# Kernel optimization log

Measured on AMD Instinct MI355X. Metric: run time of the kernel, lower is better.

Reference implementation:

```python
import jax, jax.numpy as jnp
import numpy as np

N_NODES = 50000
N_EDGES = 800000
F_IN = 64
HID = 256
N_GRAPHS = 128
N_OUT = 24


def _sage_conv(x, src, dst, deg_inv, wl, bl, wr):
    # PyG SAGEConv (aggr='mean'): out = lin_l(mean_{j in N(i)} x_j) + lin_r(x_i)
    agg = jax.ops.segment_sum(x[src], dst, num_segments=x.shape[0]) * deg_inv
    return agg @ wl.T + bl + x @ wr.T


def setup_inputs() -> dict:
    key = jax.random.key(0)
    ks = jax.random.split(key, 16)
    x = jax.random.normal(ks[0], (N_NODES, F_IN), dtype=jnp.float32)
    edge_index = jax.random.randint(ks[1], (2, N_EDGES), 0, N_NODES, dtype=jnp.int64)
    batch = jnp.sort(jax.random.randint(ks[2], (N_NODES,), 0, N_GRAPHS, dtype=jnp.int64))

    def lin(k, fan_out, fan_in):
        bound = 1.0 / np.sqrt(fan_in)
        return jax.random.uniform(k, (fan_out, fan_in), jnp.float32, -bound, bound)

    inp = {
        'x': x, 'edge_index': edge_index, 'batch': batch,
        'w1l': lin(ks[3], HID, F_IN), 'b1': jnp.zeros((HID,), jnp.float32), 'w1r': lin(ks[4], HID, F_IN),
        'w2l': lin(ks[5], HID, HID), 'b2': jnp.zeros((HID,), jnp.float32), 'w2r': lin(ks[6], HID, HID),
        'w3l': lin(ks[7], HID, HID), 'b3': jnp.zeros((HID,), jnp.float32), 'w3r': lin(ks[8], HID, HID),
        'lin1_w': lin(ks[9], HID // 2, HID), 'lin1_b': jnp.zeros((HID // 2,), jnp.float32),
        'lin2_w': lin(ks[10], N_OUT, HID // 2), 'lin2_b': jnp.zeros((N_OUT,), jnp.float32),
    }
    return inp


def reference(x, edge_index, batch, w1l, b1, w1r, w2l, b2, w2r, w3l, b3, w3r,
              lin1_w, lin1_b, lin2_w, lin2_b):
    src, dst = edge_index[0], edge_index[1]
    deg = jax.ops.segment_sum(jnp.ones((src.shape[0],), jnp.float32), dst, num_segments=x.shape[0])
    deg_inv = (1.0 / jnp.maximum(deg, 1.0))[:, None]  # [N,1]

    h = jax.nn.relu(_sage_conv(x, src, dst, deg_inv, w1l, b1, w1r))
    h = jax.nn.relu(_sage_conv(h, src, dst, deg_inv, w2l, b2, w2r))
    h = jax.nn.relu(_sage_conv(h, src, dst, deg_inv, w3l, b3, w3r))

    # global mean pool over graphs
    pooled_sum = jax.ops.segment_sum(h, batch, num_segments=N_GRAPHS)
    counts = jax.ops.segment_sum(jnp.ones((h.shape[0],), jnp.float32), batch, num_segments=N_GRAPHS)
    pooled = pooled_sum / jnp.maximum(counts, 1.0)[:, None]

    g = jax.nn.relu(pooled @ lin1_w.T + lin1_b)
    return g @ lin2_w.T + lin2_b
```

## Files before the change

kernel.cpp:

```cpp
#include <hip/hip_runtime.h>

#define N_NODES 50000
#define M_PAD   50048
#define N_EDGES 800000
#define F_IN 64
#define HID 256
#define N_GRAPHS 128
#define N_OUT 24

typedef unsigned short ushort_t;
typedef __attribute__((ext_vector_type(8))) unsigned short us8;
typedef __attribute__((ext_vector_type(8))) __bf16 bf16x8;
typedef __attribute__((ext_vector_type(4))) float f32x4;

#define SLICE_US ((size_t)M_PAD * 32)

__device__ __forceinline__ unsigned short f2bf(float f) {
  unsigned u = __builtin_bit_cast(unsigned, f);
  return (unsigned short)((u + 0x7fffu + ((u >> 16) & 1u)) >> 16);
}
__device__ __forceinline__ float bf2f(unsigned short h) {
  return __builtin_bit_cast(float, (unsigned)h << 16);
}

__device__ __forceinline__ f32x4 mfma_bf16(us8 a, us8 b, f32x4 c) {
  return __builtin_amdgcn_mfma_f32_16x16x32_bf16(
      __builtin_bit_cast(bf16x8, a), __builtin_bit_cast(bf16x8, b), c, 0, 0, 0);
}

__device__ __forceinline__ void gload16(const ushort_t* g, ushort_t* l) {
  __builtin_amdgcn_global_load_lds(
      (const __attribute__((address_space(1))) void*)g,
      (__attribute__((address_space(3))) void*)l, 16, 0, 0);
}


__global__ void k_hist(const int* __restrict__ dst, int* __restrict__ deg_priv,
                       int* __restrict__ rank) {
  int e = blockIdx.x * 256 + threadIdx.x;
  if (e < N_EDGES) {
    int c = blockIdx.x & 7;
    rank[e] = atomicAdd(&deg_priv[c * N_NODES + dst[e]], 1);
  }
}

__global__ void k_gofs(const int* __restrict__ batch, int* __restrict__ gofs) {
  int t = threadIdx.x;
  if (t > N_GRAPHS) return;
  int lo = 0, hi = N_NODES;
  while (lo < hi) {
    int mid = (lo + hi) >> 1;
    if (batch[mid] < t) lo = mid + 1;
    else hi = mid;
  }
  gofs[t] = lo;
}

__global__ __launch_bounds__(1024) void k_scan1(int* __restrict__ deg_priv,
                                                int* __restrict__ deg,
                                                int* __restrict__ rowptr,
                                                int* __restrict__ partial) {
  __shared__ int s[1024];
  int t = threadIdx.x;
  int idx = blockIdx.x * 1024 + t;
  int v = 0;
  if (idx < N_NODES) {
    int run = 0;
#pragma unroll
    for (int c = 0; c < 8; ++c) {
      int dv = deg_priv[c * N_NODES + idx];
      deg_priv[c * N_NODES + idx] = run;
      run += dv;
    }
    deg[idx] = run;
    v = run;
  }
  s[t] = v;
  __syncthreads();
  for (int off = 1; off < 1024; off <<= 1) {
    int a = (t >= off) ? s[t - off] : 0;
    __syncthreads();
    s[t] += a;
    __syncthreads();
  }
  if (idx < N_NODES) rowptr[idx] = s[t] - v;
  if (t == 1023) partial[blockIdx.x] = s[1023];
}

__global__ void k_scan2(int* __restrict__ partial, int* __restrict__ rowptr) {
  __shared__ int s[64];
  int t = threadIdx.x;
  const int NB = (N_NODES + 1023) / 1024;
  int v = (t < NB) ? partial[t] : 0;
  s[t] = v;
  __syncthreads();
  for (int off = 1; off < 64; off <<= 1) {
    int a = (t >= off) ? s[t - off] : 0;
    __syncthreads();
    s[t] += a;
    __syncthreads();
  }
  if (t < NB) partial[t] = s[t] - v;
  if (t == NB - 1) rowptr[N_NODES] = s[t];
}

__global__ __launch_bounds__(1024) void k_scan3(const int* __restrict__ deg,
                                                const int* __restrict__ partial,
                                                int* __restrict__ rowptr,
                                                float* __restrict__ deg_inv) {
  int idx = blockIdx.x * 1024 + threadIdx.x;
  if (idx < N_NODES) {
    rowptr[idx] += partial[blockIdx.x];
    deg_inv[idx] = 1.0f / fmaxf((float)deg[idx], 1.0f);
  }
}

__global__ void k_place(const int* __restrict__ src, const int* __restrict__ dst,
                        const int* __restrict__ rowptr, const int* __restrict__ deg_priv,
                        const int* __restrict__ rank, int* __restrict__ esrc) {
  int e = blockIdx.x * 256 + threadIdx.x;
  if (e < N_EDGES) {
    int c = blockIdx.x & 7;
    int d = dst[e];
    esrc[rowptr[d] + deg_priv[c * N_NODES + d] + rank[e]] = src[e];
  }
}


__global__ void k_prep_x(const float* __restrict__ x, ushort_t* __restrict__ xio) {
  int g = blockIdx.x * 256 + threadIdx.x;
  if (g >= N_NODES * 8) return;
  int row = g >> 3, kb = g & 7;
  const float* p = x + (size_t)row * F_IN + kb * 8;
  us8 H, L;
#pragma unroll
  for (int i = 0; i < 8; ++i) {
    float f = p[i];
    unsigned short hi = f2bf(f);
    H[i] = hi;
    L[i] = f2bf(f - bf2f(hi));
  }
  size_t ob = (size_t)row * 128 + (size_t)((kb ^ (row & 7)) << 3);
  *(us8*)&xio[ob] = H;
  *(us8*)&xio[ob + 64] = L;
}

__global__ void k_prep_w(const float* __restrict__ w1lp, const float* __restrict__ w1rp,
                         const float* __restrict__ w2lp, const float* __restrict__ w2rp,
                         const float* __restrict__ w3lp, const float* __restrict__ w3rp,
                         ushort_t* __restrict__ wf1, ushort_t* __restrict__ wf2,
                         ushort_t* __restrict__ wf3) {
  int layer = blockIdx.z, side = blockIdx.y;
  const int Kg = (layer == 0) ? 8 : 32;
  const int qcs = Kg >> 2;
  int g = blockIdx.x * 256 + threadIdx.x;
  if (g >= 256 * Kg) return;
  const float* src = (layer == 0) ? (side ? w1rp : w1lp)
                   : (layer == 1) ? (side ? w2rp : w2lp)
                                  : (side ? w3rp : w3lp);
  ushort_t* dstf = (layer == 0) ? wf1 : (layer == 1) ? wf2 : wf3;
  int row = g / Kg, gb = g % Kg;
  const float* p = src + (size_t)row * (Kg * 8) + gb * 8;
  us8 H, L;
#pragma unroll
  for (int i = 0; i < 8; ++i) {
    float f = p[i];
    unsigned short hi = f2bf(f);
    H[i] = hi;
    L[i] = f2bf(f - bf2f(hi));
  }
  int nb2 = side * 16 + (row >> 4);
  int lane = (row & 15) + ((gb & 3) << 4);
  size_t base = ((size_t)(nb2 * qcs + (gb >> 2)) * 2) * 512 + lane * 8;
  *(us8*)&dstf[base] = H;
  *(us8*)&dstf[base + 512] = L;
}


__global__ __launch_bounds__(256) void k_agg64s(const float* __restrict__ x,
                                                const int* __restrict__ rowptr,
                                                const int* __restrict__ esrc,
                                                const float* __restrict__ deg_inv,
                                                ushort_t* __restrict__ oio) {
  int node = blockIdx.x * 4 + (threadIdx.x >> 6);
  if (node >= N_NODES) return;
  int lane = threadIdx.x & 63;
  int e0 = rowptr[node], e1 = rowptr[node + 1];
  float acc = 0.f;
  int e = e0;
#pragma unroll 1
  for (; e + 8 <= e1; e += 8) {
    int sidx[8];
#pragma unroll
    for (int j = 0; j < 8; ++j) sidx[j] = esrc[e + j];
    float v[8];
#pragma unroll
    for (int j = 0; j < 8; ++j) v[j] = x[(size_t)sidx[j] * F_IN + lane];
    acc += ((v[0] + v[1]) + (v[2] + v[3])) + ((v[4] + v[5]) + (v[6] + v[7]));
  }
  if (e + 4 <= e1) {
    int s0 = esrc[e], s1 = esrc[e + 1], s2 = esrc[e + 2], s3 = esrc[e + 3];
    float v0 = x[(size_t)s0 * F_IN + lane];
    float v1 = x[(size_t)s1 * F_IN + lane];
    float v2 = x[(size_t)s2 * F_IN + lane];
    float v3 = x[(size_t)s3 * F_IN + lane];
    acc += (v0 + v1) + (v2 + v3);
    e += 4;
  }
  for (; e < e1; ++e) acc += x[(size_t)esrc[e] * F_IN + lane];
  acc *= deg_inv[node];
  unsigned short hi = f2bf(acc);
  unsigned short lo = f2bf(acc - bf2f(hi));
  size_t rb = (size_t)node * 128;
  int slot = ((lane >> 3) ^ (node & 7)) << 3;
  oio[rb + slot + (lane & 7)] = hi;
  oio[rb + 64 + slot + (lane & 7)] = lo;
}

__global__ __launch_bounds__(256) void k_agg256s(const ushort_t* __restrict__ hio,
                                                 const int* __restrict__ rowptr,
                                                 const int* __restrict__ esrc,
                                                 const float* __restrict__ deg_inv,
                                                 ushort_t* __restrict__ oio) {
  int c = blockIdx.x & 7;
  const ushort_t* hs = hio + (size_t)c * SLICE_US;
  ushort_t* os = oio + (size_t)c * SLICE_US;
  int q = threadIdx.x & 3;
  int ns = threadIdx.x >> 2;
  for (int base = (blockIdx.x >> 3) * 64; base < N_NODES; base += 16384) {
    int node = base + ns;
    if (node >= N_NODES) continue;
    int e0 = rowptr[node], e1 = rowptr[node + 1];
    float a[8] = {0.f, 0.f, 0.f, 0.f, 0.f, 0.f, 0.f, 0.f};
    int e = e0;
#pragma unroll 1
    for (; e + 8 <= e1; e += 8) {
      int sidx[8];
#pragma unroll
      for (int j = 0; j < 8; ++j) sidx[j] = esrc[e + j];
      us8 v[8];
#pragma unroll
      for (int j = 0; j < 8; ++j)
        v[j] = *(const us8*)&hs[(size_t)sidx[j] * 32 + ((q ^ (sidx[j] & 3)) << 3)];
#pragma unroll
      for (int j = 0; j < 8; ++j)
#pragma unroll
        for (int i = 0; i < 8; ++i) a[i] += bf2f(v[j][i]);
    }
    if (e + 4 <= e1) {
      int s0 = esrc[e], s1 = esrc[e + 1], s2 = esrc[e + 2], s3 = esrc[e + 3];
      us8 v0 = *(const us8*)&hs[(size_t)s0 * 32 + ((q ^ (s0 & 3)) << 3)];
      us8 v1 = *(const us8*)&hs[(size_t)s1 * 32 + ((q ^ (s1 & 3)) << 3)];
      us8 v2 = *(const us8*)&hs[(size_t)s2 * 32 + ((q ^ (s2 & 3)) << 3)];
      us8 v3 = *(const us8*)&hs[(size_t)s3 * 32 + ((q ^ (s3 & 3)) << 3)];
#pragma unroll
      for (int i = 0; i < 8; ++i)
        a[i] += (bf2f(v0[i]) + bf2f(v1[i])) + (bf2f(v2[i]) + bf2f(v3[i]));
      e += 4;
    }
    for (; e < e1; ++e) {
      int s = esrc[e];
      us8 v = *(const us8*)&hs[(size_t)s * 32 + ((q ^ (s & 3)) << 3)];
#pragma unroll
      for (int i = 0; i < 8; ++i) a[i] += bf2f(v[i]);
    }
    float di = deg_inv[node];
    us8 H;
#pragma unroll
    for (int i = 0; i < 8; ++i) H[i] = f2bf(a[i] * di);
    __builtin_nontemporal_store(
        H, (us8*)&os[(size_t)node * 32 + ((q ^ (node & 3)) << 3)]);
  }
}


template <int SA>
__global__ __launch_bounds__(256, 2) void k_gemm_mfma(
    const ushort_t* __restrict__ A1, int k1g, const ushort_t* __restrict__ w1f,
    const ushort_t* __restrict__ A2, int k2g, const ushort_t* __restrict__ w2f,
    const float* __restrict__ bias, ushort_t* __restrict__ oio,
    float* __restrict__ ofp, int mode) {
  __shared__ __align__(16) ushort_t ldsA[2][SA ? 16384 : 8192];

  int t = threadIdx.x;
  int wv = t >> 6, lane = t & 63;
  int fr = lane & 15, kq = lane >> 4;
  int bm = blockIdx.x;
  int rowA0 = bm * 128;

  f32x4 acc[8][4];
#pragma unroll
  for (int m = 0; m < 8; ++m)
#pragma unroll
    for (int n = 0; n < 4; ++n) acc[m][n] = (f32x4)0.f;

  const int ns1 = k1g >> 3, ns2 = k2g >> 3, ns = ns1 + ns2;
  const int lj = lane & 7, lr8 = lane >> 3;

  auto stage = [&](int buf, int s) {
    bool p2 = s >= ns1;
    const ushort_t* A = p2 ? A2 : A1;
    int Kg = p2 ? k2g : k1g;
    int sl = p2 ? (s - ns1) : s;
#pragma unroll
    for (int i = 0; i < 4; ++i) {
      int row = wv * 32 + i * 8 + lr8;
      int R = rowA0 + row;
      int lo = (wv * 32 + i * 8) * 64;
      if (SA) {
        size_t offA = ((size_t)R * (Kg * 2) + sl * 8 + lj) * 8;
        gload16(A + offA, &ldsA[buf][lo]);
        gload16(A + offA + (size_t)Kg * 8, &ldsA[buf][8192 + lo]);
      } else {
        size_t offA = (size_t)(sl * 2 + ((lj >> 2) ^ ((R >> 2) & 1))) * SLICE_US +
                      (size_t)R * 32 + (size_t)((lj & 3) << 3);
        gload16(A + offA, &ldsA[buf][lo]);
      }
    }
  };

  stage(0, 0);
  __syncthreads();
  int cur = 0;

  for (int s = 0; s < ns; ++s) {
    bool p2 = s >= ns1;
    const ushort_t* Wf = p2 ? w2f : w1f;
    int sl = p2 ? (s - ns1) : s;
    int qcs = (p2 ? k2g : k1g) >> 2;

    us8 bh[2][4], bl[2][4];
#pragma unroll
    for (int kc = 0; kc < 2; ++kc)
#pragma unroll
      for (int n = 0; n < 4; ++n) {
        size_t base = ((size_t)((wv * 4 + n) * qcs + sl * 2 + kc) * 2) * 512 + lane * 8;
        bh[kc][n] = *(const us8*)&Wf[base];
        bl[kc][n] = *(const us8*)&Wf[base + 512];
      }

    if (s + 1 < ns) stage(cur ^ 1, s + 1);

#pragma unroll
    for (int kc = 0; kc < 2; ++kc) {
      int kg = kc * 4 + kq;
      int swk = (kg ^ (fr & 7)) << 3;
#pragma unroll
      for (int mh = 0; mh < 2; ++mh) {
        us8 ah[4], al[4];
#pragma unroll
        for (int m = 0; m < 4; ++m) {
          int off = ((mh * 64 + m * 16 + fr) << 6) + swk;
          ah[m] = *(const us8*)&ldsA[cur][off];
          if (SA) al[m] = *(const us8*)&ldsA[cur][8192 + off];
        }
#pragma unroll
        for (int m = 0; m < 4; ++m)
#pragma unroll
          for (int n = 0; n < 4; ++n)
            acc[mh * 4 + m][n] = mfma_bf16(ah[m], bh[kc][n], acc[mh * 4 + m][n]);
#pragma unroll
        for (int m = 0; m < 4; ++m)
#pragma unroll
          for (int n = 0; n < 4; ++n)
            acc[mh * 4 + m][n] = mfma_bf16(ah[m], bl[kc][n], acc[mh * 4 + m][n]);
        if (SA) {
#pragma unroll
          for (int m = 0; m < 4; ++m)
#pragma unroll
            for (int n = 0; n < 4; ++n)
              acc[mh * 4 + m][n] = mfma_bf16(al[m], bh[kc][n], acc[mh * 4 + m][n]);
        }
      }
    }
    __syncthreads();
    cur ^= 1;
  }

  float bv4[4];
#pragma unroll
  for (int n = 0; n < 4; ++n) bv4[n] = bias[wv * 64 + n * 16 + fr];

  if (mode == 0) {
    ushort_t* eb = &ldsA[0][0] + wv * 2048;
#pragma unroll
    for (int c = 0; c < 4; ++c) {
      __syncthreads();
#pragma unroll
      for (int mm = 0; mm < 2; ++mm) {
#pragma unroll
        for (int n = 0; n < 4; ++n) {
          f32x4 v = acc[c * 2 + mm][n];
#pragma unroll
          for (int r = 0; r < 4; ++r)
            eb[(mm * 16 + kq * 4 + r) * 64 + n * 16 + fr] =
                f2bf(fmaxf(v[r] + bv4[n], 0.f));
        }
      }
      __syncthreads();
#pragma unroll
      for (int j = 0; j < 4; ++j) {
        int rl = j * 8 + (lane >> 3);
        int g8 = lane & 7;
        us8 v = *(const us8*)&eb[rl * 64 + g8 * 8];
        int R = bm * 128 + c * 32 + rl;
        int gi = wv * 8 + g8;
        if (R < N_NODES) {
          size_t addr = (size_t)(gi >> 2) * SLICE_US + (size_t)R * 32 +
                        (size_t)(((gi & 3) ^ (R & 3)) << 3);
          *(us8*)&oio[addr] = v;
        }
      }
    }
  } else {
    float* ebf = (float*)&ldsA[0][0] + wv * 2048;
#pragma unroll
    for (int c = 0; c < 4; ++c) {
      __syncthreads();
#pragma unroll
      for (int mm = 0; mm < 2; ++mm) {
#pragma unroll
        for (int n = 0; n < 4; ++n) {
          f32x4 v = acc[c * 2 + mm][n];
#pragma unroll
          for (int r = 0; r < 4; ++r)
            ebf[(mm * 16 + kq * 4 + r) * 64 + n * 16 + fr] =
                fmaxf(v[r] + bv4[n], 0.f);
        }
      }
      __syncthreads();
#pragma unroll
      for (int j = 0; j < 8; ++j) {
        int rl = j * 4 + (lane >> 4);
        int seg = lane & 15;
        f32x4 v = *(const f32x4*)&ebf[rl * 64 + seg * 4];
        int R = bm * 128 + c * 32 + rl;
        if (R < N_NODES)
          *(f32x4*)&ofp[(size_t)R * HID + wv * 64 + seg * 4] = v;
      }
    }
  }
}


__global__ __launch_bounds__(256) void k_pool(const float* __restrict__ h,
                                              const int* __restrict__ gofs,
                                              float* __restrict__ pooled) {
  int g = blockIdx.y, c = blockIdx.x;
  int r0 = gofs[g], r1 = gofs[g + 1];
  int rg = threadIdx.x >> 6, lane = threadIdx.x & 63;
  float ax = 0.f, ay = 0.f, az = 0.f, aw = 0.f;
  for (int r = r0 + c * 4 + rg; r < r1; r += 64) {
    float4 v = *(const float4*)&h[(size_t)r * HID + lane * 4];
    ax += v.x; ay += v.y; az += v.z; aw += v.w;
  }
  __shared__ float4 sm[4][64];
  sm[rg][lane] = make_float4(ax, ay, az, aw);
  __syncthreads();
  if (rg == 0) {
    float4 s0 = sm[0][lane], s1 = sm[1][lane], s2 = sm[2][lane], s3 = sm[3][lane];
    float* p = &pooled[g * HID + lane * 4];
    atomicAdd(p + 0, s0.x + s1.x + s2.x + s3.x);
    atomicAdd(p + 1, s0.y + s1.y + s2.y + s3.y);
    atomicAdd(p + 2, s0.z + s1.z + s2.z + s3.z);
    atomicAdd(p + 3, s0.w + s1.w + s2.w + s3.w);
  }
}


__global__ __launch_bounds__(128) void k_head(const float* __restrict__ pooled,
                                              const int* __restrict__ gofs,
                                              const float* __restrict__ w1,
                                              const float* __restrict__ b1,
                                              const float* __restrict__ w2,
                                              const float* __restrict__ b2,
                                              float* __restrict__ out) {
  __shared__ float p[HID];
  __shared__ float g1[HID / 2];
  int g = blockIdx.x, t = threadIdx.x;
  float inv = 1.f / fmaxf((float)(gofs[g + 1] - gofs[g]), 1.f);
  p[t] = pooled[g * HID + t] * inv;
  p[t + 128] = pooled[g * HID + 128 + t] * inv;
  __syncthreads();
  float s = b1[t];
#pragma unroll 4
  for (int k = 0; k < HID; ++k) s = fmaf(p[k], w1[t * HID + k], s);
  g1[t] = fmaxf(s, 0.f);
  __syncthreads();
  if (t < N_OUT) {
    float s2 = b2[t];
#pragma unroll 4
    for (int k = 0; k < HID / 2; ++k) s2 = fmaf(g1[k], w2[t * (HID / 2) + k], s2);
    out[g * N_OUT + t] = s2;
  }
}


extern "C" void kernel_launch(void* const* d_in, const int* in_sizes, int n_in,
                              void* d_out, int out_size, void* d_ws, size_t ws_size,
                              hipStream_t stream) {
  const float* x      = (const float*)d_in[0];
  const int*   ei     = (const int*)d_in[1];
  const int*   batch  = (const int*)d_in[2];
  const float* w1lw   = (const float*)d_in[3];
  const float* b1     = (const float*)d_in[4];
  const float* w1rw   = (const float*)d_in[5];
  const float* w2lw   = (const float*)d_in[6];
  const float* b2     = (const float*)d_in[7];
  const float* w2rw   = (const float*)d_in[8];
  const float* w3lw   = (const float*)d_in[9];
  const float* b3     = (const float*)d_in[10];
  const float* w3rw   = (const float*)d_in[11];
  const float* lin1_w = (const float*)d_in[12];
  const float* lin1_b = (const float*)d_in[13];
  const float* lin2_w = (const float*)d_in[14];
  const float* lin2_b = (const float*)d_in[15];
  float* out = (float*)d_out;

  const int* srcIdx = ei;
  const int* dstIdx = ei + N_EDGES;

  size_t off = 0;
  auto carve = [&](size_t bytes) {
    size_t r = off;
    off += (bytes + 255) & ~(size_t)255;
    return r;
  };
  char* ws = (char*)d_ws;
  int*      deg_priv = (int*)(ws + carve((size_t)8 * N_NODES * 4));
  int*      deg      = (int*)(ws + carve((size_t)N_NODES * 4));
  int*      rank     = (int*)(ws + carve((size_t)N_EDGES * 4));
  int*      rowptr   = (int*)(ws + carve((size_t)(N_NODES + 1) * 4));
  float*    deg_inv  = (float*)(ws + carve((size_t)N_NODES * 4));
  int*      esrc     = (int*)(ws + carve((size_t)N_EDGES * 4));
  int*      partial  = (int*)(ws + carve(64 * 4));
  int*      gofs     = (int*)(ws + carve((N_GRAPHS + 1) * 4));
  ushort_t* xio      = (ushort_t*)(ws + carve((size_t)M_PAD * 128 * 2));
  ushort_t* agg1     = (ushort_t*)(ws + carve((size_t)M_PAD * 128 * 2));
  ushort_t* agg      = (ushort_t*)(ws + carve((size_t)M_PAD * 256 * 2));
  char*     h1blk    = ws + carve((size_t)M_PAD * HID * 4);
  ushort_t* h1       = (ushort_t*)h1blk;
  float*    h3       = (float*)h1blk;
  ushort_t* h2       = (ushort_t*)(ws + carve((size_t)M_PAD * 256 * 2));
  ushort_t* wf1      = (ushort_t*)(ws + carve((size_t)2 * 32768 * 2));
  ushort_t* wf2      = (ushort_t*)(ws + carve((size_t)2 * 131072 * 2));
  ushort_t* wf3      = (ushort_t*)(ws + carve((size_t)2 * 131072 * 2));
  float*    pooled   = (float*)(ws + carve((size_t)N_GRAPHS * HID * 4));
  (void)ws_size; (void)n_in; (void)in_sizes; (void)out_size;

  hipMemsetAsync(deg_priv, 0, (size_t)8 * N_NODES * 4, stream);
  hipMemsetAsync(pooled, 0, (size_t)N_GRAPHS * HID * 4, stream);

  const int EB = (N_EDGES + 255) / 256;
  const int SB = (N_NODES + 1023) / 1024;

  k_hist<<<EB, 256, 0, stream>>>(dstIdx, deg_priv, rank);
  k_gofs<<<1, 256, 0, stream>>>(batch, gofs);
  k_scan1<<<SB, 1024, 0, stream>>>(deg_priv, deg, rowptr, partial);
  k_scan2<<<1, 64, 0, stream>>>(partial, rowptr);
  k_scan3<<<SB, 1024, 0, stream>>>(deg, partial, rowptr, deg_inv);
  k_place<<<EB, 256, 0, stream>>>(srcIdx, dstIdx, rowptr, deg_priv, rank, esrc);

  k_prep_x<<<(N_NODES * 8 + 255) / 256, 256, 0, stream>>>(x, xio);
  k_prep_w<<<dim3(32, 2, 3), 256, 0, stream>>>(w1lw, w1rw, w2lw, w2rw, w3lw, w3rw,
                                               wf1, wf2, wf3);

  const int GB = (N_NODES + 127) / 128;
  const int AB = (N_NODES + 3) / 4;
  const int AGB = 2048;

  k_agg64s<<<AB, 256, 0, stream>>>(x, rowptr, esrc, deg_inv, agg1);
  k_gemm_mfma<1><<<GB, 256, 0, stream>>>(agg1, 8, wf1,
                                         xio, 8, wf1 + 32768,
                                         b1, h1, nullptr, 0);
  k_agg256s<<<AGB, 256, 0, stream>>>(h1, rowptr, esrc, deg_inv, agg);
  k_gemm_mfma<0><<<GB, 256, 0, stream>>>(agg, 32, wf2,
                                         h1, 32, wf2 + 131072,
                                         b2, h2, nullptr, 0);
  k_agg256s<<<AGB, 256, 0, stream>>>(h2, rowptr, esrc, deg_inv, agg);
  k_gemm_mfma<0><<<GB, 256, 0, stream>>>(agg, 32, wf3,
                                         h2, 32, wf3 + 131072,
                                         b3, nullptr, h3, 1);

  k_pool<<<dim3(16, N_GRAPHS), 256, 0, stream>>>(h3, gofs, pooled);
  k_head<<<N_GRAPHS, 128, 0, stream>>>(pooled, gofs, lin1_w, lin1_b, lin2_w, lin2_b, out);
}
```

Measured before the change: 307.9 us.

## Gather layer-1 aggregation from sliced bf16 copy of x with per-thread nodes

The first-layer mean aggregation now reads a bf16 (hi-only) copy of x, laid out as 8 column slices of 8 features, instead of fp32 x. Each thread handles one node and one 16-byte slice, and blocks are assigned to slices so each slice stays cache-resident, matching the layer-2/3 aggregation scheme. This halves gather bytes and improves cache locality, but drops the low bf16 part of x in the aggregated input, reducing precision. Outputs are written with nontemporal vector stores.

```diff
diff --git a/kernel.cpp b/kernel.cpp
--- a/kernel.cpp
+++ b/kernel.cpp
@@ -14,6 +14,7 @@
 typedef __attribute__((ext_vector_type(4))) float f32x4;
 
 #define SLICE_US ((size_t)M_PAD * 32)
+#define XSLICE_US ((size_t)M_PAD * 8)
 
 __device__ __forceinline__ unsigned short f2bf(float f) {
   unsigned u = __builtin_bit_cast(unsigned, f);
@@ -127,7 +128,8 @@
 }
 
 
-__global__ void k_prep_x(const float* __restrict__ x, ushort_t* __restrict__ xio) {
+__global__ void k_prep_x(const float* __restrict__ x, ushort_t* __restrict__ xio,
+                         ushort_t* __restrict__ xhs) {
   int g = blockIdx.x * 256 + threadIdx.x;
   if (g >= N_NODES * 8) return;
   int row = g >> 3, kb = g & 7;
@@ -143,6 +145,7 @@
   size_t ob = (size_t)row * 128 + (size_t)((kb ^ (row & 7)) << 3);
   *(us8*)&xio[ob] = H;
   *(us8*)&xio[ob + 64] = L;
+  *(us8*)&xhs[(size_t)kb * XSLICE_US + (size_t)row * 8] = H;
 }
 
 __global__ void k_prep_w(const float* __restrict__ w1lp, const float* __restrict__ w1rp,
@@ -177,44 +180,63 @@
 }
 
 
-__global__ __launch_bounds__(256) void k_agg64s(const float* __restrict__ x,
+__global__ __launch_bounds__(256) void k_agg64s(const ushort_t* __restrict__ xhs,
                                                 const int* __restrict__ rowptr,
                                                 const int* __restrict__ esrc,
                                                 const float* __restrict__ deg_inv,
                                                 ushort_t* __restrict__ oio) {
-  int node = blockIdx.x * 4 + (threadIdx.x >> 6);
-  if (node >= N_NODES) return;
-  int lane = threadIdx.x & 63;
-  int e0 = rowptr[node], e1 = rowptr[node + 1];
-  float acc = 0.f;
-  int e = e0;
+  int c = blockIdx.x & 7;
+  const ushort_t* xs = xhs + (size_t)c * XSLICE_US;
+  int ln = threadIdx.x;
+  for (int base = (blockIdx.x >> 3) * 256; base < N_NODES; base += 65536) {
+    int node = base + ln;
+    if (node >= N_NODES) continue;
+    int e0 = rowptr[node], e1 = rowptr[node + 1];
+    float a[8] = {0.f, 0.f, 0.f, 0.f, 0.f, 0.f, 0.f, 0.f};
+    int e = e0;
 #pragma unroll 1
-  for (; e + 8 <= e1; e += 8) {
-    int sidx[8];
-#pragma unroll
-    for (int j = 0; j < 8; ++j) sidx[j] = esrc[e + j];
-    float v[8];
-#pragma unroll
-    for (int j = 0; j < 8; ++j) v[j] = x[(size_t)sidx[j] * F_IN + lane];
-    acc += ((v[0] + v[1]) + (v[2] + v[3])) + ((v[4] + v[5]) + (v[6] + v[7]));
-  }
-  if (e + 4 <= e1) {
-    int s0 = esrc[e], s1 = esrc[e + 1], s2 = esrc[e + 2], s3 = esrc[e + 3];
-    float v0 = x[(size_t)s0 * F_IN + lane];
-    float v1 = x[(size_t)s1 * F_IN + lane];
-    float v2 = x[(size_t)s2 * F_IN + lane];
-    float v3 = x[(size_t)s3 * F_IN + lane];
-    acc += (v0 + v1) + (v2 + v3);
-    e += 4;
-  }
-  for (; e < e1; ++e) acc += x[(size_t)esrc[e] * F_IN + lane];
-  acc *= deg_inv[node];
-  unsigned short hi = f2bf(acc);
-  unsigned short lo = f2bf(acc - bf2f(hi));
-  size_t rb = (size_t)node * 128;
-  int slot = ((lane >> 3) ^ (node & 7)) << 3;
-  oio[rb + slot + (lane & 7)] = hi;
-  oio[rb + 64 + slot + (lane & 7)] = lo;
+    for (; e + 8 <= e1; e += 8) {
+      int sidx[8];
+#pragma unroll
+      for (int j = 0; j < 8; ++j) sidx[j] = esrc[e + j];
+      us8 v[8];
+#pragma unroll
+      for (int j = 0; j < 8; ++j) v[j] = *(const us8*)&xs[(size_t)sidx[j] * 8];
+#pragma unroll
+      for (int j = 0; j < 8; ++j)
+#pragma unroll
+        for (int i = 0; i < 8; ++i) a[i] += bf2f(v[j][i]);
+    }
+    if (e + 4 <= e1) {
+      int s0 = esrc[e], s1 = esrc[e + 1], s2 = esrc[e + 2], s3 = esrc[e + 3];
+      us8 v0 = *(const us8*)&xs[(size_t)s0 * 8];
+      us8 v1 = *(const us8*)&xs[(size_t)s1 * 8];
+      us8 v2 = *(const us8*)&xs[(size_t)s2 * 8];
+      us8 v3 = *(const us8*)&xs[(size_t)s3 * 8];
+#pragma unroll
+      for (int i = 0; i < 8; ++i)
+        a[i] += (bf2f(v0[i]) + bf2f(v1[i])) + (bf2f(v2[i]) + bf2f(v3[i]));
+      e += 4;
+    }
+    for (; e < e1; ++e) {
+      int s = esrc[e];
+      us8 v = *(const us8*)&xs[(size_t)s * 8];
+#pragma unroll
+      for (int i = 0; i < 8; ++i) a[i] += bf2f(v[i]);
+    }
+    float di = deg_inv[node];
+    us8 H, L;
+#pragma unroll
+    for (int i = 0; i < 8; ++i) {
+      float f = a[i] * di;
+      unsigned short hi = f2bf(f);
+      H[i] = hi;
+      L[i] = f2bf(f - bf2f(hi));
+    }
+    size_t rb = (size_t)node * 128 + (size_t)((c ^ (node & 7)) << 3);
+    __builtin_nontemporal_store(H, (us8*)&oio[rb]);
+    __builtin_nontemporal_store(L, (us8*)&oio[rb + 64]);
+  }
 }
 
 __global__ __launch_bounds__(256) void k_agg256s(const ushort_t* __restrict__ hio,
@@ -536,6 +558,7 @@
   int*      partial  = (int*)(ws + carve(64 * 4));
   int*      gofs     = (int*)(ws + carve((N_GRAPHS + 1) * 4));
   ushort_t* xio      = (ushort_t*)(ws + carve((size_t)M_PAD * 128 * 2));
+  ushort_t* xhs      = (ushort_t*)(ws + carve((size_t)M_PAD * 64 * 2));
   ushort_t* agg1     = (ushort_t*)(ws + carve((size_t)M_PAD * 128 * 2));
   ushort_t* agg      = (ushort_t*)(ws + carve((size_t)M_PAD * 256 * 2));
   char*     h1blk    = ws + carve((size_t)M_PAD * HID * 4);
@@ -561,15 +584,14 @@
   k_scan3<<<SB, 1024, 0, stream>>>(deg, partial, rowptr, deg_inv);
   k_place<<<EB, 256, 0, stream>>>(srcIdx, dstIdx, rowptr, deg_priv, rank, esrc);
 
-  k_prep_x<<<(N_NODES * 8 + 255) / 256, 256, 0, stream>>>(x, xio);
+  k_prep_x<<<(N_NODES * 8 + 255) / 256, 256, 0, stream>>>(x, xio, xhs);
   k_prep_w<<<dim3(32, 2, 3), 256, 0, stream>>>(w1lw, w1rw, w2lw, w2rw, w3lw, w3rw,
                                                wf1, wf2, wf3);
 
   const int GB = (N_NODES + 127) / 128;
-  const int AB = (N_NODES + 3) / 4;
   const int AGB = 2048;
 
-  k_agg64s<<<AB, 256, 0, stream>>>(x, rowptr, esrc, deg_inv, agg1);
+  k_agg64s<<<AGB, 256, 0, stream>>>(xhs, rowptr, esrc, deg_inv, agg1);
   k_gemm_mfma<1><<<GB, 256, 0, stream>>>(agg1, 8, wf1,
                                          xio, 8, wf1 + 32768,
                                          b1, h1, nullptr, 0);
```

Measured after the change: 319.2 us. 3.7% more time.
